# Kernel optimization log

Measured on AMD Instinct MI355X. Metric: run time of the kernel, lower is better.

## Reference

```python
import jax, jax.numpy as jnp
import numpy as np

DIM = 512
HEADS = 8
DIM_HEAD = 64
INNER = HEADS * DIM_HEAD  # 512
LN_EPS = 1e-5


def setup_inputs() -> dict:
    key = jax.random.key(0)
    ks = jax.random.split(key, 6)
    b, n = 2, 2048
    x = jax.random.normal(ks[0], (b, n, DIM), dtype=jnp.float32)
    # to_qkv: Linear(dim, inner*3, bias=False); torch weight is [out,in], apply as x @ W.T
    w_qkv = jax.random.normal(ks[1], (3 * INNER, DIM), dtype=jnp.float32) * (DIM ** -0.5)
    reattn_w = jax.random.normal(ks[2], (HEADS, HEADS), dtype=jnp.float32)
    ln_g = jnp.ones((HEADS,), dtype=jnp.float32)
    ln_b = jnp.zeros((HEADS,), dtype=jnp.float32)
    w_out = jax.random.normal(ks[3], (DIM, INNER), dtype=jnp.float32) * (INNER ** -0.5)
    b_out = jnp.zeros((DIM,), dtype=jnp.float32)
    return {"x": x, "w_qkv": w_qkv, "reattn_w": reattn_w,
            "ln_g": ln_g, "ln_b": ln_b, "w_out": w_out, "b_out": b_out}


def reference(x, w_qkv, reattn_w, ln_g, ln_b, w_out, b_out):
    b, n, _ = x.shape
    scale = DIM_HEAD ** -0.5
    qkv = x @ w_qkv.T  # [b, n, 3*inner]
    q, k, v = jnp.split(qkv, 3, axis=-1)
    # b n (h d) -> b h n d
    split_heads = lambda t: t.reshape(b, n, HEADS, DIM_HEAD).transpose(0, 2, 1, 3)
    q, k, v = split_heads(q), split_heads(k), split_heads(v)
    dots = jnp.einsum('bhid,bhjd->bhij', q, k) * scale
    attn = jax.nn.softmax(dots, axis=-1)
    # re-attention: cross-head mixing then LayerNorm over head dim
    attn = jnp.einsum('bhij,hg->bgij', attn, reattn_w)
    a = attn.transpose(0, 2, 3, 1)  # b i j h
    mu = jnp.mean(a, axis=-1, keepdims=True)
    var = jnp.mean((a - mu) ** 2, axis=-1, keepdims=True)
    a = (a - mu) * jax.lax.rsqrt(var + LN_EPS) * ln_g + ln_b
    attn = a.transpose(0, 3, 1, 2)  # b h i j
    out = jnp.einsum('bhij,bhjd->bhid', attn, v)
    out = out.transpose(0, 2, 1, 3).reshape(b, n, INNER)
    out = out @ w_out.T + b_out  # dropout p=0 -> identity
    return out
```

## Files before the change

### kernel.cpp

```cpp
#include <hip/hip_runtime.h>
#include <hip/hip_bf16.h>


typedef __attribute__((ext_vector_type(8))) short bfx8;
typedef __attribute__((ext_vector_type(4))) float f32x4;
typedef unsigned short u16;
typedef unsigned int u32;

#define QSCALE 0.18033688011112042f

static __device__ inline u16 f2bf(float f) {
  union { float f; unsigned u; } cv; cv.f = f;
  unsigned u = cv.u;
  u += 0x7fffu + ((u >> 16) & 1u);
  return (u16)(u >> 16);
}
static __device__ inline u32 cvtpk(float lo, float hi) {
  u32 d; asm("v_cvt_pk_bf16_f32 %0, %1, %2" : "=v"(d) : "v"(lo), "v"(hi)); return d;
}
static __device__ inline float fexp2(float x) {
  float r; asm("v_exp_f32 %0, %1" : "=v"(r) : "v"(x)); return r;
}
static __device__ inline float flog2(float x) {
  float r; asm("v_log_f32 %0, %1" : "=v"(r) : "v"(x)); return r;
}

__global__ __launch_bounds__(256) void convert3(
    const float* __restrict__ x, const float* __restrict__ wq,
    const float* __restrict__ wo,
    u16* __restrict__ xb, u16* __restrict__ wqb, u16* __restrict__ wob) {
  int e = (blockIdx.x * 256 + threadIdx.x) * 4;
  const float* src; u16* dst; int off;
  if (e < 2097152)      { src = x;  dst = xb;  off = e; }
  else if (e < 2883584) { src = wq; dst = wqb; off = e - 2097152; }
  else                  { src = wo; dst = wob; off = e - 2883584; }
  float4 v = *(const float4*)&src[off];
  ushort4 o; o.x = f2bf(v.x); o.y = f2bf(v.y); o.z = f2bf(v.z); o.w = f2bf(v.w);
  *(ushort4*)&dst[off] = o;
}

__global__ __launch_bounds__(256) void gemm_qkv(
    const u16* __restrict__ A, const u16* __restrict__ B,
    u16* __restrict__ qb, u16* __restrict__ kb, u16* __restrict__ vtb) {
  __shared__ u16 As[128 * 32];
  __shared__ u16 Bs[128 * 32];
  const int t = threadIdx.x, lane = t & 63;
  const int wm = (t >> 6) >> 1, wn = (t >> 6) & 1;
  const int m0 = blockIdx.y * 128, n0 = blockIdx.x * 128;
  const int li = lane & 15, lg = lane >> 4;
  const int rowA = t >> 2, kb8 = (t & 3) * 8;
  f32x4 acc[4][4] = {};
  for (int k0 = 0; k0 < 512; k0 += 32) {
    __syncthreads();
    *(bfx8*)&As[rowA * 32 + kb8]        = *(const bfx8*)&A[(size_t)(m0 + rowA) * 512 + k0 + kb8];
    *(bfx8*)&As[(rowA + 64) * 32 + kb8] = *(const bfx8*)&A[(size_t)(m0 + rowA + 64) * 512 + k0 + kb8];
    *(bfx8*)&Bs[rowA * 32 + kb8]        = *(const bfx8*)&B[(size_t)(n0 + rowA) * 512 + k0 + kb8];
    *(bfx8*)&Bs[(rowA + 64) * 32 + kb8] = *(const bfx8*)&B[(size_t)(n0 + rowA + 64) * 512 + k0 + kb8];
    __syncthreads();
    bfx8 af[4], bf_[4];
#pragma unroll
    for (int mi = 0; mi < 4; mi++)
      af[mi] = *(const bfx8*)&As[(wm * 64 + mi * 16 + li) * 32 + lg * 8];
#pragma unroll
    for (int ni = 0; ni < 4; ni++)
      bf_[ni] = *(const bfx8*)&Bs[(wn * 64 + ni * 16 + li) * 32 + lg * 8];
#pragma unroll
    for (int mi = 0; mi < 4; mi++)
#pragma unroll
      for (int ni = 0; ni < 4; ni++)
        acc[mi][ni] = __builtin_amdgcn_mfma_f32_16x16x32_bf16(af[mi], bf_[ni], acc[mi][ni], 0, 0, 0);
  }
#pragma unroll
  for (int mi = 0; mi < 4; mi++) {
#pragma unroll
    for (int ni = 0; ni < 4; ni++) {
      const int nc  = n0 + wn * 64 + ni * 16 + li;
      const int mrb = m0 + wm * 64 + mi * 16 + lg * 4;
      const int part = nc >> 9, within = nc & 511;
      const int h = within >> 6, d = within & 63;
      const int bb = mrb >> 11, ii = mrb & 2047;
      if (part == 0) {
#pragma unroll
        for (int r = 0; r < 4; r++)
          qb[(((size_t)bb * 8 + h) * 2048 + ii + r) * 64 + d] = f2bf(acc[mi][ni][r] * QSCALE);
      } else if (part == 1) {
#pragma unroll
        for (int r = 0; r < 4; r++)
          kb[(((size_t)bb * 8 + h) * 2048 + ii + r) * 64 + d] = f2bf(acc[mi][ni][r]);
      } else {
        ushort4 u;
        u.x = f2bf(acc[mi][ni][0]); u.y = f2bf(acc[mi][ni][1]);
        u.z = f2bf(acc[mi][ni][2]); u.w = f2bf(acc[mi][ni][3]);
        *(ushort4*)&vtb[(((size_t)bb * 8 + h) * 64 + d) * 2048 + ii] = u;
      }
    }
  }
}

__global__ __launch_bounds__(256) void passA(
    const u16* __restrict__ qb, const u16* __restrict__ kb,
    float2* __restrict__ statp) {
  const int t = threadIdx.x, lane = t & 63, w = t >> 6;
  const int bh = blockIdx.y, js = blockIdx.z;
  const int i0 = blockIdx.x * 64 + w * 16;
  const int li = lane & 15, lg = lane >> 4;
  const u16* Qh = qb + ((size_t)bh * 2048 + i0 + li) * 64;
  const u16* Kb = kb + (size_t)bh * 2048 * 64;
  const bfx8 q0 = *(const bfx8*)&Qh[lg * 8];
  const bfx8 q1 = *(const bfx8*)&Qh[32 + lg * 8];
  float m = -1e30f, l = 0.f;
  const int jbeg = js * 512, jend = jbeg + 512;
  for (int j0 = jbeg; j0 < jend; j0 += 32) {
    const u16* KhA = Kb + (size_t)(j0 + li) * 64;
    const u16* KhB = KhA + 16 * 64;
    bfx8 a0 = *(const bfx8*)&KhA[lg * 8];
    bfx8 a1 = *(const bfx8*)&KhA[32 + lg * 8];
    bfx8 b0 = *(const bfx8*)&KhB[lg * 8];
    bfx8 b1 = *(const bfx8*)&KhB[32 + lg * 8];
    __builtin_amdgcn_sched_barrier(0);
    f32x4 sa = {0.f, 0.f, 0.f, 0.f}, sb = {0.f, 0.f, 0.f, 0.f};
    sa = __builtin_amdgcn_mfma_f32_16x16x32_bf16(a0, q0, sa, 0, 0, 0);
    sa = __builtin_amdgcn_mfma_f32_16x16x32_bf16(a1, q1, sa, 0, 0, 0);
    sb = __builtin_amdgcn_mfma_f32_16x16x32_bf16(b0, q0, sb, 0, 0, 0);
    sb = __builtin_amdgcn_mfma_f32_16x16x32_bf16(b1, q1, sb, 0, 0, 0);
    float mt = fmaxf(fmaxf(fmaxf(sa[0], sa[1]), fmaxf(sa[2], sa[3])),
                     fmaxf(fmaxf(sb[0], sb[1]), fmaxf(sb[2], sb[3])));
    float mn = fmaxf(m, mt);
    float es = (fexp2(sa[0] - mn) + fexp2(sa[1] - mn)) + (fexp2(sa[2] - mn) + fexp2(sa[3] - mn))
             + (fexp2(sb[0] - mn) + fexp2(sb[1] - mn)) + (fexp2(sb[2] - mn) + fexp2(sb[3] - mn));
    l = fmaf(l, fexp2(m - mn), es);
    m = mn;
  }
  for (int off = 16; off < 64; off <<= 1) {
    float mo = __shfl_xor(m, off, 64);
    float lo = __shfl_xor(l, off, 64);
    float mn = fmaxf(m, mo);
    l = l * fexp2(m - mn) + lo * fexp2(mo - mn);
    m = mn;
  }
  if (lane < 16) statp[(size_t)js * 32768 + (size_t)bh * 2048 + i0 + li] = make_float2(m, l);
}

__global__ __launch_bounds__(512) __attribute__((amdgpu_waves_per_eu(4, 4)))
void passB(
    const u16* __restrict__ qb, const u16* __restrict__ kb,
    const u16* __restrict__ vtb, const float2* __restrict__ statp,
    const float* __restrict__ Wmix, const float* __restrict__ lng,
    const float* __restrict__ lnb, u16* __restrict__ innerP) {
  __shared__ __align__(16) u16 A2[8 * 16 * 128];
  __shared__ __align__(16) u16 Qs[8 * 16 * 72];
  const int t = threadIdx.x, lane = t & 63, w = t >> 6;
  const int b = blockIdx.y, i0 = blockIdx.x * 16;
  const int li = lane & 15, lg = lane >> 4;
  const int swz = (li & 7) << 3;

#pragma unroll
  for (int cc = 0; cc < 2; cc++) {
    const int c = t + cc * 512;
    const int h = c >> 7, qi = (c >> 3) & 15, d8 = c & 7;
    bfx8 v = *(const bfx8*)&qb[(((size_t)(b * 8 + h)) * 2048 + i0 + qi) * 64 + d8 * 8];
    *(bfx8*)&Qs[(h * 16 + qi) * 72 + d8 * 8] = v;
  }

  float wm_[8][8], lng_[8], lnb_[8];
#pragma unroll
  for (int h = 0; h < 8; h++)
#pragma unroll
    for (int g = 0; g < 8; g++) wm_[h][g] = Wmix[h * 8 + g];
#pragma unroll
  for (int g = 0; g < 8; g++) { lng_[g] = lng[g]; lnb_[g] = lnb[g]; }

  float stM[8];
#pragma unroll
  for (int h = 0; h < 8; h++) {
    const size_t idx = ((size_t)(b * 8 + h)) * 2048 + i0 + li;
    float m = -1e30f, l = 0.f;
#pragma unroll
    for (int z = 0; z < 4; z++) {
      const float2 a = statp[(size_t)z * 32768 + idx];
      const float mn = fmaxf(m, a.x);
      l = l * fexp2(m - mn) + a.y * fexp2(a.x - mn);
      m = mn;
    }
    stM[h] = m + flog2(l);
  }

  __syncthreads();

  f32x4 pacc[4] = {};
  const int jmb = blockIdx.z * 1024;
  const size_t hstr = (size_t)2048 * 64;
  for (int jm = jmb; jm < jmb + 1024; jm += 128) {
    const int j0 = jm + w * 16;
    const u16* Kb0 = kb + ((size_t)(b * 8) * 2048 + j0 + li) * 64;
    float p[8][4];
#pragma unroll
    for (int hb = 0; hb < 2; hb++) {
      bfx8 kf[4][2];
#pragma unroll
      for (int hh = 0; hh < 4; hh++) {
        const u16* Kh = Kb0 + (size_t)(hb * 4 + hh) * hstr;
        kf[hh][0] = *(const bfx8*)&Kh[lg * 8];
        kf[hh][1] = *(const bfx8*)&Kh[32 + lg * 8];
      }
      __builtin_amdgcn_sched_barrier(0);
#pragma unroll
      for (int hh = 0; hh < 4; hh++) {
        const int h = hb * 4 + hh;
        const bfx8 qA = *(const bfx8*)&Qs[(h * 16 + li) * 72 + lg * 8];
        const bfx8 qB = *(const bfx8*)&Qs[(h * 16 + li) * 72 + 32 + lg * 8];
        f32x4 s = {0.f, 0.f, 0.f, 0.f};
        s = __builtin_amdgcn_mfma_f32_16x16x32_bf16(kf[hh][0], qA, s, 0, 0, 0);
        s = __builtin_amdgcn_mfma_f32_16x16x32_bf16(kf[hh][1], qB, s, 0, 0, 0);
#pragma unroll
        for (int r = 0; r < 4; r++) p[h][r] = fexp2(s[r] - stM[h]);
      }
    }
    u32 apk[8][2];
#pragma unroll
    for (int r = 0; r < 4; r++) {
      float a_[8]; float sum = 0.f, sumsq = 0.f;
#pragma unroll
      for (int g = 0; g < 8; g++) {
        float acc = 0.f;
#pragma unroll
        for (int h = 0; h < 8; h++) acc = fmaf(p[h][r], wm_[h][g], acc);
        a_[g] = acc; sum += acc; sumsq = fmaf(acc, acc, sumsq);
      }
      const float mu = sum * 0.125f;
      const float var = fmaf(sumsq, 0.125f, -mu * mu);
      const float rs = rsqrtf(var + 1e-5f);
#pragma unroll
      for (int g = 0; g < 8; g++) {
        const float av = fmaf((a_[g] - mu) * rs, lng_[g], lnb_[g]);
        if (r & 1) apk[g][r >> 1] |= cvtpk(av, av) & 0xffff0000u;
        else       apk[g][r >> 1]  = cvtpk(av, av) & 0x0000ffffu;
      }
    }
    {
      const int jsw = (w * 16 + lg * 4) ^ swz;
#pragma unroll
      for (int g = 0; g < 8; g++)
        *(uint2*)&A2[(g * 16 + li) * 128 + jsw] = make_uint2(apk[g][0], apk[g][1]);
    }
    const u16* Vh = vtb + ((size_t)(b * 8 + w)) * 64 * 2048 + jm;
    bfx8 vF[4][4];
#pragma unroll
    for (int kc = 0; kc < 4; kc++)
#pragma unroll
      for (int nd = 0; nd < 4; nd++)
        vF[kc][nd] = *(const bfx8*)&Vh[(size_t)(nd * 16 + li) * 2048 + kc * 32 + lg * 8];
    __syncthreads();
    __builtin_amdgcn_s_setprio(1);
#pragma unroll
    for (int kc = 0; kc < 4; kc++) {
      const bfx8 af = *(const bfx8*)&A2[(w * 16 + li) * 128 + ((kc * 32 + lg * 8) ^ swz)];
#pragma unroll
      for (int nd = 0; nd < 4; nd++)
        pacc[nd] = __builtin_amdgcn_mfma_f32_16x16x32_bf16(af, vF[kc][nd], pacc[nd], 0, 0, 0);
    }
    __builtin_amdgcn_s_setprio(0);
    __syncthreads();
  }
  u16* dst = innerP + (size_t)blockIdx.z * 2097152 + ((size_t)b * 2048 + i0) * 512 + w * 64;
#pragma unroll
  for (int nd = 0; nd < 4; nd++)
#pragma unroll
    for (int r = 0; r < 4; r++)
      dst[(lg * 4 + r) * 512 + nd * 16 + li] = f2bf(pacc[nd][r]);
}

static __device__ inline bfx8 addbf8(bfx8 a, bfx8 b) {
  bfx8 r;
#pragma unroll
  for (int e = 0; e < 8; e += 2) {
    union { float f; u32 u; } a0, a1, b0, b1;
    a0.u = ((u32)(u16)a[e]) << 16;     b0.u = ((u32)(u16)b[e]) << 16;
    a1.u = ((u32)(u16)a[e + 1]) << 16; b1.u = ((u32)(u16)b[e + 1]) << 16;
    const u32 pk = cvtpk(a0.f + b0.f, a1.f + b1.f);
    r[e] = (short)(pk & 0xffff); r[e + 1] = (short)(pk >> 16);
  }
  return r;
}

__global__ __launch_bounds__(256) void gemm_out(
    const u16* __restrict__ A0, const u16* __restrict__ A1,
    const u16* __restrict__ B,
    float* __restrict__ outf, const float* __restrict__ bias) {
  __shared__ u16 As[128 * 32];
  __shared__ u16 Bs[128 * 32];
  const int t = threadIdx.x, lane = t & 63;
  const int wm = (t >> 6) >> 1, wn = (t >> 6) & 1;
  const int m0 = blockIdx.y * 128, n0 = blockIdx.x * 128;
  const int li = lane & 15, lg = lane >> 4;
  const int rowA = t >> 2, kb8 = (t & 3) * 8;
  f32x4 acc[4][4] = {};
  for (int k0 = 0; k0 < 512; k0 += 32) {
    __syncthreads();
    {
      const size_t iA = (size_t)(m0 + rowA) * 512 + k0 + kb8;
      const size_t iB = (size_t)(m0 + rowA + 64) * 512 + k0 + kb8;
      *(bfx8*)&As[rowA * 32 + kb8] =
          addbf8(*(const bfx8*)&A0[iA], *(const bfx8*)&A1[iA]);
      *(bfx8*)&As[(rowA + 64) * 32 + kb8] =
          addbf8(*(const bfx8*)&A0[iB], *(const bfx8*)&A1[iB]);
      *(bfx8*)&Bs[rowA * 32 + kb8]        = *(const bfx8*)&B[(size_t)(n0 + rowA) * 512 + k0 + kb8];
      *(bfx8*)&Bs[(rowA + 64) * 32 + kb8] = *(const bfx8*)&B[(size_t)(n0 + rowA + 64) * 512 + k0 + kb8];
    }
    __syncthreads();
    bfx8 af[4], bf_[4];
#pragma unroll
    for (int mi = 0; mi < 4; mi++)
      af[mi] = *(const bfx8*)&As[(wm * 64 + mi * 16 + li) * 32 + lg * 8];
#pragma unroll
    for (int ni = 0; ni < 4; ni++)
      bf_[ni] = *(const bfx8*)&Bs[(wn * 64 + ni * 16 + li) * 32 + lg * 8];
#pragma unroll
    for (int mi = 0; mi < 4; mi++)
#pragma unroll
      for (int ni = 0; ni < 4; ni++)
        acc[mi][ni] = __builtin_amdgcn_mfma_f32_16x16x32_bf16(af[mi], bf_[ni], acc[mi][ni], 0, 0, 0);
  }
#pragma unroll
  for (int mi = 0; mi < 4; mi++) {
#pragma unroll
    for (int ni = 0; ni < 4; ni++) {
      const int nc  = n0 + wn * 64 + ni * 16 + li;
      const int mrb = m0 + wm * 64 + mi * 16 + lg * 4;
      const float bv = bias[nc];
#pragma unroll
      for (int r = 0; r < 4; r++)
        outf[(size_t)(mrb + r) * 512 + nc] = acc[mi][ni][r] + bv;
    }
  }
}

extern "C" void kernel_launch(void* const* d_in, const int* in_sizes, int n_in,
                              void* d_out, int out_size, void* d_ws, size_t ws_size,
                              hipStream_t stream) {
  const float* x      = (const float*)d_in[0];
  const float* w_qkv  = (const float*)d_in[1];
  const float* reattn = (const float*)d_in[2];
  const float* ln_g   = (const float*)d_in[3];
  const float* ln_b   = (const float*)d_in[4];
  const float* w_out  = (const float*)d_in[5];
  const float* b_out  = (const float*)d_in[6];
  float* out = (float*)d_out;
  char* ws = (char*)d_ws;
  u16*    xb    = (u16*)(ws + 0);
  u16*    wqb   = (u16*)(ws + 4194304);
  u16*    innerP= (u16*)(ws + 0);
  u16*    qbf   = (u16*)(ws + 8388608);
  u16*    kbf   = (u16*)(ws + 12582912);
  u16*    vtb   = (u16*)(ws + 16777216);
  float2* statp = (float2*)(ws + 20971520);
  u16*    wob   = (u16*)(ws + 22020096);

  convert3<<<3072, 256, 0, stream>>>(x, w_qkv, w_out, xb, wqb, wob);
  gemm_qkv<<<dim3(12, 32), 256, 0, stream>>>(xb, wqb, qbf, kbf, vtb);
  passA<<<dim3(32, 16, 4), 256, 0, stream>>>(qbf, kbf, statp);
  passB<<<dim3(128, 2, 2), 512, 0, stream>>>(qbf, kbf, vtb, statp, reattn, ln_g, ln_b, innerP);
  gemm_out<<<dim3(4, 32), 256, 0, stream>>>(innerP, innerP + 2097152, wob, out, b_out);
}
```

Before: 227.9 us.

## Split passB into 4 key chunks with fp32 atomic reduction and packed FMA mixing

passB now runs 256-thread blocks over four key-range splits instead of 512 threads over two. Each wave handles two output heads by reloading V fragments, and the head-mixing plus LayerNorm math uses packed v_pk_fma_f32 pair operations. Partial outputs are combined with fp32 atomicAdd into a zeroed buffer, then a new convert kernel casts them to bf16 for gemm_out, so gemm_out no longer adds two bf16 partials. This adds a memset, an extra kernel launch and atomic traffic in exchange for more blocks and lower per-thread VALU work.

New measurement: 246.6 us. 1.08x slower.

```diff
diff --git a/kernel.cpp b/kernel.cpp
--- a/kernel.cpp
+++ b/kernel.cpp
@@ -4,6 +4,7 @@
 
 typedef __attribute__((ext_vector_type(8))) short bfx8;
 typedef __attribute__((ext_vector_type(4))) float f32x4;
+typedef __attribute__((ext_vector_type(2))) float f32x2;
 typedef unsigned short u16;
 typedef unsigned int u32;
 
@@ -141,13 +142,13 @@
   if (lane < 16) statp[(size_t)js * 32768 + (size_t)bh * 2048 + i0 + li] = make_float2(m, l);
 }
 
-__global__ __launch_bounds__(512) __attribute__((amdgpu_waves_per_eu(4, 4)))
+__global__ __launch_bounds__(256) __attribute__((amdgpu_waves_per_eu(3)))
 void passB(
     const u16* __restrict__ qb, const u16* __restrict__ kb,
     const u16* __restrict__ vtb, const float2* __restrict__ statp,
     const float* __restrict__ Wmix, const float* __restrict__ lng,
-    const float* __restrict__ lnb, u16* __restrict__ innerP) {
-  __shared__ __align__(16) u16 A2[8 * 16 * 128];
+    const float* __restrict__ lnb, float* __restrict__ innerF) {
+  __shared__ __align__(16) u16 A2[8 * 16 * 72];
   __shared__ __align__(16) u16 Qs[8 * 16 * 72];
   const int t = threadIdx.x, lane = t & 63, w = t >> 6;
   const int b = blockIdx.y, i0 = blockIdx.x * 16;
@@ -155,20 +156,26 @@
   const int swz = (li & 7) << 3;
 
 #pragma unroll
-  for (int cc = 0; cc < 2; cc++) {
-    const int c = t + cc * 512;
+  for (int cc = 0; cc < 4; cc++) {
+    const int c = t + cc * 256;
     const int h = c >> 7, qi = (c >> 3) & 15, d8 = c & 7;
     bfx8 v = *(const bfx8*)&qb[(((size_t)(b * 8 + h)) * 2048 + i0 + qi) * 64 + d8 * 8];
     *(bfx8*)&Qs[(h * 16 + qi) * 72 + d8 * 8] = v;
   }
 
-  float wm_[8][8], lng_[8], lnb_[8];
+  f32x2 wm2_[8][4], lg2_[4], lb2_[4];
 #pragma unroll
   for (int h = 0; h < 8; h++)
 #pragma unroll
-    for (int g = 0; g < 8; g++) wm_[h][g] = Wmix[h * 8 + g];
-#pragma unroll
-  for (int g = 0; g < 8; g++) { lng_[g] = lng[g]; lnb_[g] = lnb[g]; }
+    for (int gp = 0; gp < 4; gp++) {
+      wm2_[h][gp][0] = Wmix[h * 8 + gp * 2];
+      wm2_[h][gp][1] = Wmix[h * 8 + gp * 2 + 1];
+    }
+#pragma unroll
+  for (int gp = 0; gp < 4; gp++) {
+    lg2_[gp][0] = lng[gp * 2]; lg2_[gp][1] = lng[gp * 2 + 1];
+    lb2_[gp][0] = lnb[gp * 2]; lb2_[gp][1] = lnb[gp * 2 + 1];
+  }
 
   float stM[8];
 #pragma unroll
@@ -187,10 +194,10 @@
 
   __syncthreads();
 
-  f32x4 pacc[4] = {};
-  const int jmb = blockIdx.z * 1024;
+  f32x4 pacc[2][4] = {};
+  const int jmb = blockIdx.z * 512;
   const size_t hstr = (size_t)2048 * 64;
-  for (int jm = jmb; jm < jmb + 1024; jm += 128) {
+  for (int jm = jmb; jm < jmb + 512; jm += 64) {
     const int j0 = jm + w * 16;
     const u16* Kb0 = kb + ((size_t)(b * 8) * 2048 + j0 + li) * 64;
     float p[8][4];
@@ -217,75 +224,101 @@
       }
     }
     u32 apk[8][2];
+    float tmp[8];
 #pragma unroll
     for (int r = 0; r < 4; r++) {
-      float a_[8]; float sum = 0.f, sumsq = 0.f;
-#pragma unroll
-      for (int g = 0; g < 8; g++) {
-        float acc = 0.f;
-#pragma unroll
-        for (int h = 0; h < 8; h++) acc = fmaf(p[h][r], wm_[h][g], acc);
-        a_[g] = acc; sum += acc; sumsq = fmaf(acc, acc, sumsq);
-      }
+      f32x2 a2g[4] = {{0.f, 0.f}, {0.f, 0.f}, {0.f, 0.f}, {0.f, 0.f}};
+#pragma unroll
+      for (int h = 0; h < 8; h++) {
+        f32x2 pb; pb[0] = p[h][r]; pb[1] = p[h][r];
+#pragma unroll
+        for (int gp = 0; gp < 4; gp++)
+          asm("v_pk_fma_f32 %0, %1, %2, %0" : "+v"(a2g[gp]) : "s"(wm2_[h][gp]), "v"(pb));
+      }
+      f32x2 sum2 = (a2g[0] + a2g[1]) + (a2g[2] + a2g[3]);
+      f32x2 sq2 = a2g[0] * a2g[0] + a2g[1] * a2g[1];
+      sq2 = sq2 + a2g[2] * a2g[2] + a2g[3] * a2g[3];
+      const float sum = sum2[0] + sum2[1];
+      const float sumsq = sq2[0] + sq2[1];
       const float mu = sum * 0.125f;
       const float var = fmaf(sumsq, 0.125f, -mu * mu);
       const float rs = rsqrtf(var + 1e-5f);
-#pragma unroll
-      for (int g = 0; g < 8; g++) {
-        const float av = fmaf((a_[g] - mu) * rs, lng_[g], lnb_[g]);
-        if (r & 1) apk[g][r >> 1] |= cvtpk(av, av) & 0xffff0000u;
-        else       apk[g][r >> 1]  = cvtpk(av, av) & 0x0000ffffu;
+      f32x2 mu2; mu2[0] = mu; mu2[1] = mu;
+      f32x2 rs2; rs2[0] = rs; rs2[1] = rs;
+#pragma unroll
+      for (int gp = 0; gp < 4; gp++) {
+        f32x2 av = (a2g[gp] - mu2) * rs2;
+        av = av * lg2_[gp] + lb2_[gp];
+        if (r & 1) {
+          apk[gp * 2][r >> 1]     = cvtpk(tmp[gp * 2], av[0]);
+          apk[gp * 2 + 1][r >> 1] = cvtpk(tmp[gp * 2 + 1], av[1]);
+        } else {
+          tmp[gp * 2] = av[0]; tmp[gp * 2 + 1] = av[1];
+        }
       }
     }
     {
       const int jsw = (w * 16 + lg * 4) ^ swz;
 #pragma unroll
       for (int g = 0; g < 8; g++)
-        *(uint2*)&A2[(g * 16 + li) * 128 + jsw] = make_uint2(apk[g][0], apk[g][1]);
-    }
-    const u16* Vh = vtb + ((size_t)(b * 8 + w)) * 64 * 2048 + jm;
-    bfx8 vF[4][4];
-#pragma unroll
-    for (int kc = 0; kc < 4; kc++)
-#pragma unroll
-      for (int nd = 0; nd < 4; nd++)
-        vF[kc][nd] = *(const bfx8*)&Vh[(size_t)(nd * 16 + li) * 2048 + kc * 32 + lg * 8];
-    __syncthreads();
-    __builtin_amdgcn_s_setprio(1);
-#pragma unroll
-    for (int kc = 0; kc < 4; kc++) {
-      const bfx8 af = *(const bfx8*)&A2[(w * 16 + li) * 128 + ((kc * 32 + lg * 8) ^ swz)];
-#pragma unroll
-      for (int nd = 0; nd < 4; nd++)
-        pacc[nd] = __builtin_amdgcn_mfma_f32_16x16x32_bf16(af, vF[kc][nd], pacc[nd], 0, 0, 0);
-    }
-    __builtin_amdgcn_s_setprio(0);
-    __syncthreads();
-  }
-  u16* dst = innerP + (size_t)blockIdx.z * 2097152 + ((size_t)b * 2048 + i0) * 512 + w * 64;
-#pragma unroll
-  for (int nd = 0; nd < 4; nd++)
-#pragma unroll
-    for (int r = 0; r < 4; r++)
-      dst[(lg * 4 + r) * 512 + nd * 16 + li] = f2bf(pacc[nd][r]);
-}
-
-static __device__ inline bfx8 addbf8(bfx8 a, bfx8 b) {
-  bfx8 r;
-#pragma unroll
-  for (int e = 0; e < 8; e += 2) {
-    union { float f; u32 u; } a0, a1, b0, b1;
-    a0.u = ((u32)(u16)a[e]) << 16;     b0.u = ((u32)(u16)b[e]) << 16;
-    a1.u = ((u32)(u16)a[e + 1]) << 16; b1.u = ((u32)(u16)b[e + 1]) << 16;
-    const u32 pk = cvtpk(a0.f + b0.f, a1.f + b1.f);
-    r[e] = (short)(pk & 0xffff); r[e + 1] = (short)(pk >> 16);
-  }
-  return r;
+        *(uint2*)&A2[(g * 16 + li) * 72 + jsw] = make_uint2(apk[g][0], apk[g][1]);
+    }
+    bfx8 vF[2][4];
+    {
+      const u16* Vh = vtb + ((size_t)(b * 8 + w)) * 64 * 2048 + jm;
+#pragma unroll
+      for (int kc = 0; kc < 2; kc++)
+#pragma unroll
+        for (int nd = 0; nd < 4; nd++)
+          vF[kc][nd] = *(const bfx8*)&Vh[(size_t)(nd * 16 + li) * 2048 + kc * 32 + lg * 8];
+    }
+    __syncthreads();
+#pragma unroll
+    for (int hh = 0; hh < 2; hh++) {
+      const int hd = w + hh * 4;
+      if (hh == 1) {
+        const u16* Vh = vtb + ((size_t)(b * 8 + hd)) * 64 * 2048 + jm;
+#pragma unroll
+        for (int kc = 0; kc < 2; kc++)
+#pragma unroll
+          for (int nd = 0; nd < 4; nd++)
+            vF[kc][nd] = *(const bfx8*)&Vh[(size_t)(nd * 16 + li) * 2048 + kc * 32 + lg * 8];
+        __builtin_amdgcn_sched_barrier(0);
+      }
+      __builtin_amdgcn_s_setprio(1);
+#pragma unroll
+      for (int kc = 0; kc < 2; kc++) {
+        const bfx8 af = *(const bfx8*)&A2[(hd * 16 + li) * 72 + ((kc * 32 + lg * 8) ^ swz)];
+#pragma unroll
+        for (int nd = 0; nd < 4; nd++)
+          pacc[hh][nd] = __builtin_amdgcn_mfma_f32_16x16x32_bf16(af, vF[kc][nd], pacc[hh][nd], 0, 0, 0);
+      }
+      __builtin_amdgcn_s_setprio(0);
+    }
+    __syncthreads();
+  }
+#pragma unroll
+  for (int hh = 0; hh < 2; hh++) {
+    const int hd = w + hh * 4;
+#pragma unroll
+    for (int nd = 0; nd < 4; nd++)
+#pragma unroll
+      for (int r = 0; r < 4; r++)
+        atomicAdd(&innerF[((size_t)b * 2048 + i0 + lg * 4 + r) * 512 + hd * 64 + nd * 16 + li],
+                  pacc[hh][nd][r]);
+  }
+}
+
+__global__ __launch_bounds__(256) void convertInner(
+    const float* __restrict__ inF, u16* __restrict__ outB) {
+  int e = (blockIdx.x * 256 + threadIdx.x) * 4;
+  float4 v = *(const float4*)&inF[e];
+  ushort4 o; o.x = f2bf(v.x); o.y = f2bf(v.y); o.z = f2bf(v.z); o.w = f2bf(v.w);
+  *(ushort4*)&outB[e] = o;
 }
 
 __global__ __launch_bounds__(256) void gemm_out(
-    const u16* __restrict__ A0, const u16* __restrict__ A1,
-    const u16* __restrict__ B,
+    const u16* __restrict__ A, const u16* __restrict__ B,
     float* __restrict__ outf, const float* __restrict__ bias) {
   __shared__ u16 As[128 * 32];
   __shared__ u16 Bs[128 * 32];
@@ -297,16 +330,10 @@
   f32x4 acc[4][4] = {};
   for (int k0 = 0; k0 < 512; k0 += 32) {
     __syncthreads();
-    {
-      const size_t iA = (size_t)(m0 + rowA) * 512 + k0 + kb8;
-      const size_t iB = (size_t)(m0 + rowA + 64) * 512 + k0 + kb8;
-      *(bfx8*)&As[rowA * 32 + kb8] =
-          addbf8(*(const bfx8*)&A0[iA], *(const bfx8*)&A1[iA]);
-      *(bfx8*)&As[(rowA + 64) * 32 + kb8] =
-          addbf8(*(const bfx8*)&A0[iB], *(const bfx8*)&A1[iB]);
-      *(bfx8*)&Bs[rowA * 32 + kb8]        = *(const bfx8*)&B[(size_t)(n0 + rowA) * 512 + k0 + kb8];
-      *(bfx8*)&Bs[(rowA + 64) * 32 + kb8] = *(const bfx8*)&B[(size_t)(n0 + rowA + 64) * 512 + k0 + kb8];
-    }
+    *(bfx8*)&As[rowA * 32 + kb8]        = *(const bfx8*)&A[(size_t)(m0 + rowA) * 512 + k0 + kb8];
+    *(bfx8*)&As[(rowA + 64) * 32 + kb8] = *(const bfx8*)&A[(size_t)(m0 + rowA + 64) * 512 + k0 + kb8];
+    *(bfx8*)&Bs[rowA * 32 + kb8]        = *(const bfx8*)&B[(size_t)(n0 + rowA) * 512 + k0 + kb8];
+    *(bfx8*)&Bs[(rowA + 64) * 32 + kb8] = *(const bfx8*)&B[(size_t)(n0 + rowA + 64) * 512 + k0 + kb8];
     __syncthreads();
     bfx8 af[4], bf_[4];
 #pragma unroll
@@ -349,16 +376,19 @@
   char* ws = (char*)d_ws;
   u16*    xb    = (u16*)(ws + 0);
   u16*    wqb   = (u16*)(ws + 4194304);
-  u16*    innerP= (u16*)(ws + 0);
+  float*  innerF= (float*)(ws + 0);
   u16*    qbf   = (u16*)(ws + 8388608);
   u16*    kbf   = (u16*)(ws + 12582912);
   u16*    vtb   = (u16*)(ws + 16777216);
   float2* statp = (float2*)(ws + 20971520);
   u16*    wob   = (u16*)(ws + 22020096);
+  u16*    innerB= (u16*)(ws + 8388608);
 
   convert3<<<3072, 256, 0, stream>>>(x, w_qkv, w_out, xb, wqb, wob);
   gemm_qkv<<<dim3(12, 32), 256, 0, stream>>>(xb, wqb, qbf, kbf, vtb);
+  hipMemsetAsync(innerF, 0, 8388608, stream);
   passA<<<dim3(32, 16, 4), 256, 0, stream>>>(qbf, kbf, statp);
-  passB<<<dim3(128, 2, 2), 512, 0, stream>>>(qbf, kbf, vtb, statp, reattn, ln_g, ln_b, innerP);
-  gemm_out<<<dim3(4, 32), 256, 0, stream>>>(innerP, innerP + 2097152, wob, out, b_out);
-}
+  passB<<<dim3(128, 2, 4), 256, 0, stream>>>(qbf, kbf, vtb, statp, reattn, ln_g, ln_b, innerF);
+  convertInner<<<2048, 256, 0, stream>>>(innerF, innerB);
+  gemm_out<<<dim3(4, 32), 256, 0, stream>>>(innerB, wob, out, b_out);
+}
```

## Split passB key range across waves with register accumulators and LDS reduction

Applied to the files above, without the earlier changes.

passB now gives each wave a contiguous 256-key slice for all 8 heads and accumulates P·V in registers with 16x16x16 MFMAs fed directly from packed registers. This removes the per-iteration LDS staging of the attention tile and the two block barriers per step. The partial sums from the 8 waves are then reduced through LDS at the end. The separate blockIdx.z split and the extra bf16 partial buffer are dropped, so gemm_out no longer adds two inputs. In exchange the grid halves to 256 blocks, register pressure rises (occupancy hint lowered to 2 waves/EU), and the V loads become narrow strided 8-byte global reads.

New measurement: 291.7 us. +28.0%, slower.

```diff
diff --git a/kernel.cpp b/kernel.cpp
--- a/kernel.cpp
+++ b/kernel.cpp
@@ -3,6 +3,7 @@
 
 
 typedef __attribute__((ext_vector_type(8))) short bfx8;
+typedef __attribute__((ext_vector_type(4))) short bfx4;
 typedef __attribute__((ext_vector_type(4))) float f32x4;
 typedef unsigned short u16;
 typedef unsigned int u32;
@@ -23,6 +24,14 @@
 }
 static __device__ inline float flog2(float x) {
   float r; asm("v_log_f32 %0, %1" : "=v"(r) : "v"(x)); return r;
+}
+static __device__ inline f32x4 mfma16(bfx4 a, bfx4 b, f32x4 c) {
+#if __has_builtin(__builtin_amdgcn_mfma_f32_16x16x16bf16_1k)
+  return __builtin_amdgcn_mfma_f32_16x16x16bf16_1k(a, b, c, 0, 0, 0);
+#else
+  asm("v_mfma_f32_16x16x16_bf16 %0, %1, %2, %0" : "+v"(c) : "v"(a), "v"(b));
+  return c;
+#endif
 }
 
 __global__ __launch_bounds__(256) void convert3(
@@ -141,18 +150,17 @@
   if (lane < 16) statp[(size_t)js * 32768 + (size_t)bh * 2048 + i0 + li] = make_float2(m, l);
 }
 
-__global__ __launch_bounds__(512) __attribute__((amdgpu_waves_per_eu(4, 4)))
+__global__ __launch_bounds__(512) __attribute__((amdgpu_waves_per_eu(2, 2)))
 void passB(
     const u16* __restrict__ qb, const u16* __restrict__ kb,
     const u16* __restrict__ vtb, const float2* __restrict__ statp,
     const float* __restrict__ Wmix, const float* __restrict__ lng,
-    const float* __restrict__ lnb, u16* __restrict__ innerP) {
-  __shared__ __align__(16) u16 A2[8 * 16 * 128];
+    const float* __restrict__ lnb, u16* __restrict__ inner) {
   __shared__ __align__(16) u16 Qs[8 * 16 * 72];
+  __shared__ __align__(16) float Red[8 * 64 * 36];
   const int t = threadIdx.x, lane = t & 63, w = t >> 6;
   const int b = blockIdx.y, i0 = blockIdx.x * 16;
   const int li = lane & 15, lg = lane >> 4;
-  const int swz = (li & 7) << 3;
 
 #pragma unroll
   for (int cc = 0; cc < 2; cc++) {
@@ -187,11 +195,10 @@
 
   __syncthreads();
 
-  f32x4 pacc[4] = {};
-  const int jmb = blockIdx.z * 1024;
+  f32x4 pacc[8][4] = {};
   const size_t hstr = (size_t)2048 * 64;
-  for (int jm = jmb; jm < jmb + 1024; jm += 128) {
-    const int j0 = jm + w * 16;
+  const int jb = w * 256;
+  for (int j0 = jb; j0 < jb + 256; j0 += 16) {
     const u16* Kb0 = kb + ((size_t)(b * 8) * 2048 + j0 + li) * 64;
     float p[8][4];
 #pragma unroll
@@ -217,6 +224,7 @@
       }
     }
     u32 apk[8][2];
+    float tmp[8];
 #pragma unroll
     for (int r = 0; r < 4; r++) {
       float a_[8]; float sum = 0.f, sumsq = 0.f;
@@ -233,59 +241,54 @@
 #pragma unroll
       for (int g = 0; g < 8; g++) {
         const float av = fmaf((a_[g] - mu) * rs, lng_[g], lnb_[g]);
-        if (r & 1) apk[g][r >> 1] |= cvtpk(av, av) & 0xffff0000u;
-        else       apk[g][r >> 1]  = cvtpk(av, av) & 0x0000ffffu;
-      }
-    }
+        if (r & 1) apk[g][r >> 1] = cvtpk(tmp[g], av);
+        else       tmp[g] = av;
+      }
+    }
+#pragma unroll
+    for (int h = 0; h < 8; h++) {
+      const u16* Vh = vtb + ((size_t)(b * 8 + h)) * 64 * 2048 + j0 + lg * 4;
+      union { u32 u[2]; bfx4 v; } bu;
+      bu.u[0] = apk[h][0]; bu.u[1] = apk[h][1];
+#pragma unroll
+      for (int dt = 0; dt < 4; dt++) {
+        const bfx4 va = *(const bfx4*)&Vh[(size_t)(dt * 16 + li) * 2048];
+        pacc[h][dt] = mfma16(va, bu.v, pacc[h][dt]);
+      }
+    }
+  }
+
+#pragma unroll
+  for (int hc = 0; hc < 4; hc++) {
+    __syncthreads();
+#pragma unroll
+    for (int hh = 0; hh < 2; hh++)
+#pragma unroll
+      for (int dt = 0; dt < 4; dt++)
+        *(f32x4*)&Red[((size_t)w * 64 + lane) * 36 + (hh * 4 + dt) * 4] =
+            pacc[hc * 2 + hh][dt];
+    __syncthreads();
     {
-      const int jsw = (w * 16 + lg * 4) ^ swz;
-#pragma unroll
-      for (int g = 0; g < 8; g++)
-        *(uint2*)&A2[(g * 16 + li) * 128 + jsw] = make_uint2(apk[g][0], apk[g][1]);
-    }
-    const u16* Vh = vtb + ((size_t)(b * 8 + w)) * 64 * 2048 + jm;
-    bfx8 vF[4][4];
-#pragma unroll
-    for (int kc = 0; kc < 4; kc++)
-#pragma unroll
-      for (int nd = 0; nd < 4; nd++)
-        vF[kc][nd] = *(const bfx8*)&Vh[(size_t)(nd * 16 + li) * 2048 + kc * 32 + lg * 8];
-    __syncthreads();
-    __builtin_amdgcn_s_setprio(1);
-#pragma unroll
-    for (int kc = 0; kc < 4; kc++) {
-      const bfx8 af = *(const bfx8*)&A2[(w * 16 + li) * 128 + ((kc * 32 + lg * 8) ^ swz)];
-#pragma unroll
-      for (int nd = 0; nd < 4; nd++)
-        pacc[nd] = __builtin_amdgcn_mfma_f32_16x16x32_bf16(af, vF[kc][nd], pacc[nd], 0, 0, 0);
-    }
-    __builtin_amdgcn_s_setprio(0);
-    __syncthreads();
-  }
-  u16* dst = innerP + (size_t)blockIdx.z * 2097152 + ((size_t)b * 2048 + i0) * 512 + w * 64;
-#pragma unroll
-  for (int nd = 0; nd < 4; nd++)
-#pragma unroll
-    for (int r = 0; r < 4; r++)
-      dst[(lg * 4 + r) * 512 + nd * 16 + li] = f2bf(pacc[nd][r]);
-}
-
-static __device__ inline bfx8 addbf8(bfx8 a, bfx8 b) {
-  bfx8 r;
-#pragma unroll
-  for (int e = 0; e < 8; e += 2) {
-    union { float f; u32 u; } a0, a1, b0, b1;
-    a0.u = ((u32)(u16)a[e]) << 16;     b0.u = ((u32)(u16)b[e]) << 16;
-    a1.u = ((u32)(u16)a[e + 1]) << 16; b1.u = ((u32)(u16)b[e + 1]) << 16;
-    const u32 pk = cvtpk(a0.f + b0.f, a1.f + b1.f);
-    r[e] = (short)(pk & 0xffff); r[e + 1] = (short)(pk >> 16);
-  }
-  return r;
+      const int sl = t >> 3;
+      const int rg = (t & 7) * 4;
+      float4 s = {0.f, 0.f, 0.f, 0.f};
+#pragma unroll
+      for (int wv = 0; wv < 8; wv++) {
+        const float4 v = *(const float4*)&Red[((size_t)wv * 64 + sl) * 36 + rg];
+        s.x += v.x; s.y += v.y; s.z += v.z; s.w += v.w;
+      }
+      const int hh = (t >> 2) & 1, dt = t & 3;
+      const int sli = (t >> 3) & 15, slg = t >> 7;
+      const int h = hc * 2 + hh;
+      u16* dst = inner + ((size_t)b * 2048 + i0 + sli) * 512 + h * 64 + dt * 16 + slg * 4;
+      uint2 pk; pk.x = cvtpk(s.x, s.y); pk.y = cvtpk(s.z, s.w);
+      *(uint2*)dst = pk;
+    }
+  }
 }
 
 __global__ __launch_bounds__(256) void gemm_out(
-    const u16* __restrict__ A0, const u16* __restrict__ A1,
-    const u16* __restrict__ B,
+    const u16* __restrict__ A, const u16* __restrict__ B,
     float* __restrict__ outf, const float* __restrict__ bias) {
   __shared__ u16 As[128 * 32];
   __shared__ u16 Bs[128 * 32];
@@ -297,16 +300,10 @@
   f32x4 acc[4][4] = {};
   for (int k0 = 0; k0 < 512; k0 += 32) {
     __syncthreads();
-    {
-      const size_t iA = (size_t)(m0 + rowA) * 512 + k0 + kb8;
-      const size_t iB = (size_t)(m0 + rowA + 64) * 512 + k0 + kb8;
-      *(bfx8*)&As[rowA * 32 + kb8] =
-          addbf8(*(const bfx8*)&A0[iA], *(const bfx8*)&A1[iA]);
-      *(bfx8*)&As[(rowA + 64) * 32 + kb8] =
-          addbf8(*(const bfx8*)&A0[iB], *(const bfx8*)&A1[iB]);
-      *(bfx8*)&Bs[rowA * 32 + kb8]        = *(const bfx8*)&B[(size_t)(n0 + rowA) * 512 + k0 + kb8];
-      *(bfx8*)&Bs[(rowA + 64) * 32 + kb8] = *(const bfx8*)&B[(size_t)(n0 + rowA + 64) * 512 + k0 + kb8];
-    }
+    *(bfx8*)&As[rowA * 32 + kb8]        = *(const bfx8*)&A[(size_t)(m0 + rowA) * 512 + k0 + kb8];
+    *(bfx8*)&As[(rowA + 64) * 32 + kb8] = *(const bfx8*)&A[(size_t)(m0 + rowA + 64) * 512 + k0 + kb8];
+    *(bfx8*)&Bs[rowA * 32 + kb8]        = *(const bfx8*)&B[(size_t)(n0 + rowA) * 512 + k0 + kb8];
+    *(bfx8*)&Bs[(rowA + 64) * 32 + kb8] = *(const bfx8*)&B[(size_t)(n0 + rowA + 64) * 512 + k0 + kb8];
     __syncthreads();
     bfx8 af[4], bf_[4];
 #pragma unroll
@@ -349,7 +346,7 @@
   char* ws = (char*)d_ws;
   u16*    xb    = (u16*)(ws + 0);
   u16*    wqb   = (u16*)(ws + 4194304);
-  u16*    innerP= (u16*)(ws + 0);
+  u16*    inner = (u16*)(ws + 0);
   u16*    qbf   = (u16*)(ws + 8388608);
   u16*    kbf   = (u16*)(ws + 12582912);
   u16*    vtb   = (u16*)(ws + 16777216);
@@ -359,6 +356,6 @@
   convert3<<<3072, 256, 0, stream>>>(x, w_qkv, w_out, xb, wqb, wob);
   gemm_qkv<<<dim3(12, 32), 256, 0, stream>>>(xb, wqb, qbf, kbf, vtb);
   passA<<<dim3(32, 16, 4), 256, 0, stream>>>(qbf, kbf, statp);
-  passB<<<dim3(128, 2, 2), 512, 0, stream>>>(qbf, kbf, vtb, statp, reattn, ln_g, ln_b, innerP);
-  gemm_out<<<dim3(4, 32), 256, 0, stream>>>(innerP, innerP + 2097152, wob, out, b_out);
-}
+  passB<<<dim3(128, 2), 512, 0, stream>>>(qbf, kbf, vtb, statp, reattn, ln_g, ln_b, inner);
+  gemm_out<<<dim3(4, 32), 256, 0, stream>>>(inner, wob, out, b_out);
+}
```

## Split passB key range three ways with fp32 atomic reduction and extra convert pass

Applied to the files above, without the earlier changes.

The passB grid's key dimension is split into three uneven chunks (6/5/5 tiles of 128) instead of two halves, and partial outputs are accumulated via fp32 atomicAdd into a zeroed buffer instead of writing two bf16 partials that gemm_out summed. A separate convert kernel turns the fp32 sum into bf16 before the output GEMM, which no longer performs the add. The change also raises waves_per_eu to 6, XOR-swizzles the Q tile in LDS instead of padding it, packs bf16 pairs with a single cvt, and splits V loading into two halves to reduce register pressure. It adds a memset, a conversion launch and atomic traffic in exchange for more parallel blocks and higher occupancy.

New measurement: 257.4 us. +12.9%, slower.

```diff
diff --git a/kernel.cpp b/kernel.cpp
--- a/kernel.cpp
+++ b/kernel.cpp
@@ -141,14 +141,14 @@
   if (lane < 16) statp[(size_t)js * 32768 + (size_t)bh * 2048 + i0 + li] = make_float2(m, l);
 }
 
-__global__ __launch_bounds__(512) __attribute__((amdgpu_waves_per_eu(4, 4)))
+__global__ __launch_bounds__(512) __attribute__((amdgpu_waves_per_eu(6, 6)))
 void passB(
     const u16* __restrict__ qb, const u16* __restrict__ kb,
     const u16* __restrict__ vtb, const float2* __restrict__ statp,
     const float* __restrict__ Wmix, const float* __restrict__ lng,
-    const float* __restrict__ lnb, u16* __restrict__ innerP) {
+    const float* __restrict__ lnb, float* __restrict__ innerF) {
   __shared__ __align__(16) u16 A2[8 * 16 * 128];
-  __shared__ __align__(16) u16 Qs[8 * 16 * 72];
+  __shared__ __align__(16) u16 Qs[8 * 16 * 64];
   const int t = threadIdx.x, lane = t & 63, w = t >> 6;
   const int b = blockIdx.y, i0 = blockIdx.x * 16;
   const int li = lane & 15, lg = lane >> 4;
@@ -159,7 +159,7 @@
     const int c = t + cc * 512;
     const int h = c >> 7, qi = (c >> 3) & 15, d8 = c & 7;
     bfx8 v = *(const bfx8*)&qb[(((size_t)(b * 8 + h)) * 2048 + i0 + qi) * 64 + d8 * 8];
-    *(bfx8*)&Qs[(h * 16 + qi) * 72 + d8 * 8] = v;
+    *(bfx8*)&Qs[(h * 16 + qi) * 64 + ((d8 * 8) ^ ((qi & 7) << 3))] = v;
   }
 
   float wm_[8][8], lng_[8], lnb_[8];
@@ -188,9 +188,12 @@
   __syncthreads();
 
   f32x4 pacc[4] = {};
-  const int jmb = blockIdx.z * 1024;
+  const int nmac = (blockIdx.z == 0) ? 6 : 5;
+  const int jm0 = ((blockIdx.z == 0) ? 0 : (blockIdx.z == 1 ? 6 : 11)) * 128;
   const size_t hstr = (size_t)2048 * 64;
-  for (int jm = jmb; jm < jmb + 1024; jm += 128) {
+  const int qswz = (li & 7) << 3;
+  for (int mc = 0; mc < nmac; mc++) {
+    const int jm = jm0 + mc * 128;
     const int j0 = jm + w * 16;
     const u16* Kb0 = kb + ((size_t)(b * 8) * 2048 + j0 + li) * 64;
     float p[8][4];
@@ -207,8 +210,8 @@
 #pragma unroll
       for (int hh = 0; hh < 4; hh++) {
         const int h = hb * 4 + hh;
-        const bfx8 qA = *(const bfx8*)&Qs[(h * 16 + li) * 72 + lg * 8];
-        const bfx8 qB = *(const bfx8*)&Qs[(h * 16 + li) * 72 + 32 + lg * 8];
+        const bfx8 qA = *(const bfx8*)&Qs[(h * 16 + li) * 64 + ((lg * 8) ^ qswz)];
+        const bfx8 qB = *(const bfx8*)&Qs[(h * 16 + li) * 64 + ((32 + lg * 8) ^ qswz)];
         f32x4 s = {0.f, 0.f, 0.f, 0.f};
         s = __builtin_amdgcn_mfma_f32_16x16x32_bf16(kf[hh][0], qA, s, 0, 0, 0);
         s = __builtin_amdgcn_mfma_f32_16x16x32_bf16(kf[hh][1], qB, s, 0, 0, 0);
@@ -217,6 +220,7 @@
       }
     }
     u32 apk[8][2];
+    float tmp[8];
 #pragma unroll
     for (int r = 0; r < 4; r++) {
       float a_[8]; float sum = 0.f, sumsq = 0.f;
@@ -233,8 +237,8 @@
 #pragma unroll
       for (int g = 0; g < 8; g++) {
         const float av = fmaf((a_[g] - mu) * rs, lng_[g], lnb_[g]);
-        if (r & 1) apk[g][r >> 1] |= cvtpk(av, av) & 0xffff0000u;
-        else       apk[g][r >> 1]  = cvtpk(av, av) & 0x0000ffffu;
+        if (r & 1) apk[g][r >> 1] = cvtpk(tmp[g], av);
+        else       tmp[g] = av;
       }
     }
     {
@@ -243,49 +247,47 @@
       for (int g = 0; g < 8; g++)
         *(uint2*)&A2[(g * 16 + li) * 128 + jsw] = make_uint2(apk[g][0], apk[g][1]);
     }
+    __syncthreads();
     const u16* Vh = vtb + ((size_t)(b * 8 + w)) * 64 * 2048 + jm;
-    bfx8 vF[4][4];
-#pragma unroll
-    for (int kc = 0; kc < 4; kc++)
-#pragma unroll
-      for (int nd = 0; nd < 4; nd++)
-        vF[kc][nd] = *(const bfx8*)&Vh[(size_t)(nd * 16 + li) * 2048 + kc * 32 + lg * 8];
-    __syncthreads();
-    __builtin_amdgcn_s_setprio(1);
-#pragma unroll
-    for (int kc = 0; kc < 4; kc++) {
-      const bfx8 af = *(const bfx8*)&A2[(w * 16 + li) * 128 + ((kc * 32 + lg * 8) ^ swz)];
-#pragma unroll
-      for (int nd = 0; nd < 4; nd++)
-        pacc[nd] = __builtin_amdgcn_mfma_f32_16x16x32_bf16(af, vF[kc][nd], pacc[nd], 0, 0, 0);
-    }
-    __builtin_amdgcn_s_setprio(0);
-    __syncthreads();
-  }
-  u16* dst = innerP + (size_t)blockIdx.z * 2097152 + ((size_t)b * 2048 + i0) * 512 + w * 64;
+#pragma unroll
+    for (int kcc = 0; kcc < 2; kcc++) {
+      bfx8 vF[2][4];
+#pragma unroll
+      for (int kc = 0; kc < 2; kc++)
+#pragma unroll
+        for (int nd = 0; nd < 4; nd++)
+          vF[kc][nd] = *(const bfx8*)&Vh[(size_t)(nd * 16 + li) * 2048 + (kcc * 2 + kc) * 32 + lg * 8];
+      __builtin_amdgcn_sched_barrier(0);
+      __builtin_amdgcn_s_setprio(1);
+#pragma unroll
+      for (int kc = 0; kc < 2; kc++) {
+        const bfx8 af = *(const bfx8*)&A2[(w * 16 + li) * 128 + (((kcc * 2 + kc) * 32 + lg * 8) ^ swz)];
+#pragma unroll
+        for (int nd = 0; nd < 4; nd++)
+          pacc[nd] = __builtin_amdgcn_mfma_f32_16x16x32_bf16(af, vF[kc][nd], pacc[nd], 0, 0, 0);
+      }
+      __builtin_amdgcn_s_setprio(0);
+    }
+    __syncthreads();
+  }
 #pragma unroll
   for (int nd = 0; nd < 4; nd++)
 #pragma unroll
     for (int r = 0; r < 4; r++)
-      dst[(lg * 4 + r) * 512 + nd * 16 + li] = f2bf(pacc[nd][r]);
-}
-
-static __device__ inline bfx8 addbf8(bfx8 a, bfx8 b) {
-  bfx8 r;
-#pragma unroll
-  for (int e = 0; e < 8; e += 2) {
-    union { float f; u32 u; } a0, a1, b0, b1;
-    a0.u = ((u32)(u16)a[e]) << 16;     b0.u = ((u32)(u16)b[e]) << 16;
-    a1.u = ((u32)(u16)a[e + 1]) << 16; b1.u = ((u32)(u16)b[e + 1]) << 16;
-    const u32 pk = cvtpk(a0.f + b0.f, a1.f + b1.f);
-    r[e] = (short)(pk & 0xffff); r[e + 1] = (short)(pk >> 16);
-  }
-  return r;
+      atomicAdd(&innerF[((size_t)b * 2048 + i0 + lg * 4 + r) * 512 + w * 64 + nd * 16 + li],
+                pacc[nd][r]);
+}
+
+__global__ __launch_bounds__(256) void convertInner(
+    const float* __restrict__ inF, u16* __restrict__ outB) {
+  int e = (blockIdx.x * 256 + threadIdx.x) * 4;
+  float4 v = *(const float4*)&inF[e];
+  ushort4 o; o.x = f2bf(v.x); o.y = f2bf(v.y); o.z = f2bf(v.z); o.w = f2bf(v.w);
+  *(ushort4*)&outB[e] = o;
 }
 
 __global__ __launch_bounds__(256) void gemm_out(
-    const u16* __restrict__ A0, const u16* __restrict__ A1,
-    const u16* __restrict__ B,
+    const u16* __restrict__ A, const u16* __restrict__ B,
     float* __restrict__ outf, const float* __restrict__ bias) {
   __shared__ u16 As[128 * 32];
   __shared__ u16 Bs[128 * 32];
@@ -297,16 +299,10 @@
   f32x4 acc[4][4] = {};
   for (int k0 = 0; k0 < 512; k0 += 32) {
     __syncthreads();
-    {
-      const size_t iA = (size_t)(m0 + rowA) * 512 + k0 + kb8;
-      const size_t iB = (size_t)(m0 + rowA + 64) * 512 + k0 + kb8;
-      *(bfx8*)&As[rowA * 32 + kb8] =
-          addbf8(*(const bfx8*)&A0[iA], *(const bfx8*)&A1[iA]);
-      *(bfx8*)&As[(rowA + 64) * 32 + kb8] =
-          addbf8(*(const bfx8*)&A0[iB], *(const bfx8*)&A1[iB]);
-      *(bfx8*)&Bs[rowA * 32 + kb8]        = *(const bfx8*)&B[(size_t)(n0 + rowA) * 512 + k0 + kb8];
-      *(bfx8*)&Bs[(rowA + 64) * 32 + kb8] = *(const bfx8*)&B[(size_t)(n0 + rowA + 64) * 512 + k0 + kb8];
-    }
+    *(bfx8*)&As[rowA * 32 + kb8]        = *(const bfx8*)&A[(size_t)(m0 + rowA) * 512 + k0 + kb8];
+    *(bfx8*)&As[(rowA + 64) * 32 + kb8] = *(const bfx8*)&A[(size_t)(m0 + rowA + 64) * 512 + k0 + kb8];
+    *(bfx8*)&Bs[rowA * 32 + kb8]        = *(const bfx8*)&B[(size_t)(n0 + rowA) * 512 + k0 + kb8];
+    *(bfx8*)&Bs[(rowA + 64) * 32 + kb8] = *(const bfx8*)&B[(size_t)(n0 + rowA + 64) * 512 + k0 + kb8];
     __syncthreads();
     bfx8 af[4], bf_[4];
 #pragma unroll
@@ -349,16 +345,19 @@
   char* ws = (char*)d_ws;
   u16*    xb    = (u16*)(ws + 0);
   u16*    wqb   = (u16*)(ws + 4194304);
-  u16*    innerP= (u16*)(ws + 0);
+  float*  innerF= (float*)(ws + 0);
   u16*    qbf   = (u16*)(ws + 8388608);
   u16*    kbf   = (u16*)(ws + 12582912);
   u16*    vtb   = (u16*)(ws + 16777216);
   float2* statp = (float2*)(ws + 20971520);
   u16*    wob   = (u16*)(ws + 22020096);
+  u16*    innerB= (u16*)(ws + 8388608);
 
   convert3<<<3072, 256, 0, stream>>>(x, w_qkv, w_out, xb, wqb, wob);
   gemm_qkv<<<dim3(12, 32), 256, 0, stream>>>(xb, wqb, qbf, kbf, vtb);
+  hipMemsetAsync(innerF, 0, 8388608, stream);
   passA<<<dim3(32, 16, 4), 256, 0, stream>>>(qbf, kbf, statp);
-  passB<<<dim3(128, 2, 2), 512, 0, stream>>>(qbf, kbf, vtb, statp, reattn, ln_g, ln_b, innerP);
-  gemm_out<<<dim3(4, 32), 256, 0, stream>>>(innerP, innerP + 2097152, wob, out, b_out);
-}
+  passB<<<dim3(128, 2, 3), 512, 0, stream>>>(qbf, kbf, vtb, statp, reattn, ln_g, ln_b, innerF);
+  convertInner<<<2048, 256, 0, stream>>>(innerF, innerB);
+  gemm_out<<<dim3(4, 32), 256, 0, stream>>>(innerB, wob, out, b_out);
+}
```
